# Optimization experiments

Hardware: AMD Instinct MI355X
Metric: run time of the kernel (lower is better)

The kernel has to match this reference:

```python
import jax, jax.numpy as jnp
import numpy as np

NU, NS, NT = 200000, 100000, 100000
N = NS + NU + NT          # node order: [source items | users | target items]
D = 32                    # embedding_size
K = 3                     # graph_layer_K
DK = D * (K + 1)          # 128, concat of all propagation layers
META = 64                 # meta_dim
B = 2048                  # batch
L = 50                    # padded history length
NNZ = 2000000             # nnz of normalized adjacency


def setup_inputs() -> dict:
    key = jax.random.key(0)
    ks = jax.random.split(key, 32)
    f = lambda i, shape, s=0.05: jax.random.normal(ks[i], shape, jnp.float32) * s
    z = lambda shape: jnp.zeros(shape, jnp.float32)
    return dict(
        u=jax.random.randint(ks[0], (B,), 0, NU, jnp.int32),
        si=jax.random.randint(ks[1], (B,), 0, NS, jnp.int32),
        ti=jax.random.randint(ks[2], (B,), 0, NT, jnp.int32),
        src_seq=jax.random.randint(ks[3], (NU, L), 0, NS, jnp.int32),
        tgt_seq=jax.random.randint(ks[4], (NU, L), 0, NT, jnp.int32),
        adj_rows=jax.random.randint(ks[5], (NNZ,), 0, N, jnp.int32),
        adj_cols=jax.random.randint(ks[6], (NNZ,), 0, N, jnp.int32),
        adj_vals=jax.random.uniform(ks[7], (NNZ,), jnp.float32) * 0.1,
        user_emb=f(8, (NU, D), 0.1),
        item_s_emb=f(9, (NS, D), 0.1),
        item_t_emb=f(10, (NT, D), 0.1),
        attn_s_w1=f(11, (D, D)), attn_s_b1=z((D,)), attn_s_w2=f(12, (D, 1)),
        attn_t_w1=f(13, (D, D)), attn_t_b1=z((D,)), attn_t_w2=f(14, (D, 1)),
        dec_ss_w1=f(15, (D, META)), dec_ss_b1=z((META,)),
        dec_ss_w2=f(16, (META, DK * DK), 0.02), dec_ss_b2=z((DK * DK,)),
        dec_tt_w1=f(17, (D, META)), dec_tt_b1=z((META,)),
        dec_tt_w2=f(18, (META, DK * DK), 0.02), dec_tt_b2=z((DK * DK,)),
        mlp_s_w1=f(19, (2 * DK, 128)), mlp_s_b1=z((128,)),
        mlp_s_w2=f(20, (128, 64)), mlp_s_b2=z((64,)),
        dense_s_w=f(21, (64, 1)), dense_s_b=z((1,)),
        mlp_t_w1=f(22, (2 * DK, 128)), mlp_t_b1=z((128,)),
        mlp_t_w2=f(23, (128, 64)), mlp_t_b2=z((64,)),
        dense_t_w=f(24, (64, 1)), dense_t_b=z((1,)),
    )


def _attn_pool(seq_ids, item_emb, w1, b1, w2):
    # masked attention pooling over padded history; pad id is 0
    e = item_emb[seq_ids]                          # [B,L,D]
    h = jax.nn.relu(e @ w1 + b1)                   # attention_layer_K = 1
    logits = h @ w2                                # [B,L,1], no bias on final layer
    mask = (seq_ids == 0)[..., None].astype(e.dtype)
    att = jax.nn.softmax(logits - mask * 1e8, axis=1)
    return jnp.sum(att * e, axis=1)                # [B,D]


def _meta_decode(his, w1, b1, w2, b2, u_e):
    # meta-generated per-sample DKxDK transform applied to the user embedding
    W = (jax.nn.relu(his @ w1 + b1) @ w2 + b2).reshape(-1, DK, DK)
    return jnp.einsum('bd,bde->be', u_e, W)


def _ncf(x, w1, b1, w2, b2, dw, db):
    h = jax.nn.relu(x @ w1 + b1)
    h = jax.nn.relu(h @ w2 + b2)
    return jax.nn.sigmoid(h @ dw + db)[:, 0]


def reference(u, si, ti, src_seq, tgt_seq, adj_rows, adj_cols, adj_vals,
              user_emb, item_s_emb, item_t_emb,
              attn_s_w1, attn_s_b1, attn_s_w2, attn_t_w1, attn_t_b1, attn_t_w2,
              dec_ss_w1, dec_ss_b1, dec_ss_w2, dec_ss_b2,
              dec_tt_w1, dec_tt_b1, dec_tt_w2, dec_tt_b2,
              mlp_s_w1, mlp_s_b1, mlp_s_w2, mlp_s_b2, dense_s_w, dense_s_b,
              mlp_t_w1, mlp_t_b1, mlp_t_w2, mlp_t_b2, dense_t_w, dense_t_b):
    his_s = _attn_pool(src_seq[u], item_s_emb, attn_s_w1, attn_s_b1, attn_s_w2)
    his_t = _attn_pool(tgt_seq[u], item_t_emb, attn_t_w1, attn_t_b1, attn_t_w2)

    # 'raw' graph encoder: K hops of sparse A @ E over [item_s | user | item_t]
    emb = jnp.concatenate([item_s_emb, user_emb, item_t_emb], axis=0)  # [N,D]
    all_emb = [emb]
    for _ in range(K):
        emb = jax.ops.segment_sum(adj_vals[:, None] * emb[adj_cols], adj_rows,
                                  num_segments=N)
        all_emb.append(emb)
    all_e = jnp.concatenate(all_emb, axis=1)       # [N, DK]

    si_e = all_e[si]                               # source items: rows [0, NS)
    u_e = all_e[NS + u]                            # users: rows [NS, NS+NU)
    ti_e = all_e[NS + NU + ti]                     # target items

    u_ss = _meta_decode(his_s, dec_ss_w1, dec_ss_b1, dec_ss_w2, dec_ss_b2, u_e)
    u_tt = _meta_decode(his_t, dec_tt_w1, dec_tt_b1, dec_tt_w2, dec_tt_b2, u_e)

    pred_s = _ncf(jnp.concatenate([u_ss, si_e], -1),
                  mlp_s_w1, mlp_s_b1, mlp_s_w2, mlp_s_b2, dense_s_w, dense_s_b)
    pred_t = _ncf(jnp.concatenate([u_tt, ti_e], -1),
                  mlp_t_w1, mlp_t_b1, mlp_t_w2, mlp_t_b2, dense_t_w, dense_t_b)
    return jnp.stack([pred_s, pred_t])             # [2, B]
```

## Files before the change

### kernel.cpp

```cpp
#include <hip/hip_runtime.h>
#include <hip/hip_bf16.h>

#define NU_ 200000
#define NS_ 100000
#define NT_ 100000
#define NN_ (NS_ + NU_ + NT_)
#define D_ 32
#define DK_ 128
#define META_ 64
#define B_ 2048
#define L_ 50
#define NNZ_ 2000000
#define GK_ 8192

#define RPB_ 391
#define NB_ 1024
#define STAGE_CAP_ 4096
#define CAPA_ 1280
#define CAPB_ 512

#define SB_EMB_   6250
#define IN4_SLOT3_ 100096
#define IN4_MARKS_ 50048
#define IN4_E3C_   49152
#define IN4_TOT_  (IN4_SLOT3_ + IN4_MARKS_ + IN4_E3C_)
#define SB_INIT_  ((IN4_TOT_ + 2048 + 255) / 256)
#define SB_ATT0_  0
#define SB_W2C0_  1024
#define SB_EMB0_  2048
#define SB_INIT0_ (SB_EMB0_ + SB_EMB_)
#define SB_GRID_  (SB_INIT0_ + SB_INIT_)

#define PB_GATHER_ 192
#define PB_TOT_    (PB_GATHER_ + 1024)

#define NCF_TILE_ 16

typedef __attribute__((ext_vector_type(8))) short bf16x8;
typedef __attribute__((ext_vector_type(4))) float f32x4;

__device__ inline unsigned bfpack(float a, float b) {
    unsigned r;
    asm("v_cvt_pk_bf16_f32 %0, %1, %2" : "=v"(r) : "v"(a), "v"(b));
    return r;
}
__device__ inline float bf2f(short s) {
    return __uint_as_float(((unsigned)(unsigned short)s) << 16);
}

__global__ __launch_bounds__(256) void setup_kernel(
    const float* __restrict__ item_s, const float* __restrict__ user_e,
    const float* __restrict__ item_t, unsigned short* __restrict__ tab,
    int* __restrict__ slot3, int* __restrict__ marks ,
    float* __restrict__ E3c, int* __restrict__ bcurA, int* __restrict__ bcurB,
    const int* __restrict__ u,
    const int* __restrict__ seq_s, const int* __restrict__ seq_t,
    const float* __restrict__ aw1_s, const float* __restrict__ ab1_s,
    const float* __restrict__ aw2_s,
    const float* __restrict__ aw1_t, const float* __restrict__ ab1_t,
    const float* __restrict__ aw2_t,
    float* __restrict__ his_s, float* __restrict__ his_t,
    const float* __restrict__ dw2_s, const float* __restrict__ dw2_t,
    unsigned short* __restrict__ o_s, unsigned short* __restrict__ o_t)
{
    __shared__ float w1t[1024];
    __shared__ float b1s[32];
    __shared__ float w2s[32];
    __shared__ float att[4][64];
    __shared__ int   ids[4][52];

    int bid = blockIdx.x, t = threadIdx.x;
    if (bid < SB_W2C0_) {
        int aid = bid;
        int dom = aid >> 9;
        const int* seq = dom ? seq_t : seq_s;
        const float* emb = dom ? item_t : item_s;
        const float* w1 = dom ? aw1_t : aw1_s;
        const float* b1 = dom ? ab1_t : ab1_s;
        const float* w2 = dom ? aw2_t : aw2_s;
        float* out = dom ? his_t : his_s;

        for (int idx = t; idx < 1024; idx += 256)
            w1t[(idx & 31) * 32 + (idx >> 5)] = w1[idx];
        if (t < 32) { b1s[t] = b1[t]; w2s[t] = w2[t]; }
        __syncthreads();

        int w = t >> 6, l = t & 63;
        int b = (aid & 511) * 4 + w;
        int uid = u[b];
        int lq = (l < L_) ? l : (L_ - 1);
        int id = seq[uid * L_ + lq];
        const float4* ep = (const float4*)(emb + (size_t)id * 32);
        float4 e4[8];
        #pragma unroll
        for (int q = 0; q < 8; q++) e4[q] = ep[q];
        float acc = 0.f;
        #pragma unroll
        for (int i = 0; i < 32; i++) {
            float hi = b1s[i];
            const float4* wr = (const float4*)(w1t + i * 32);
            #pragma unroll
            for (int jq = 0; jq < 8; jq++) {
                float4 wf = wr[jq];
                hi += e4[jq].x*wf.x + e4[jq].y*wf.y + e4[jq].z*wf.z + e4[jq].w*wf.w;
            }
            acc += fmaxf(hi, 0.f) * w2s[i];
        }
        float logit = (l < L_) ? (acc - (id == 0 ? 1e8f : 0.f)) : -1e30f;
        float m = logit;
        for (int off = 32; off > 0; off >>= 1) m = fmaxf(m, __shfl_down(m, off, 64));
        m = __shfl(m, 0, 64);
        float ex = (l < L_) ? expf(logit - m) : 0.f;
        float s = ex;
        for (int off = 32; off > 0; off >>= 1) s += __shfl_down(s, off, 64);
        s = __shfl(s, 0, 64);
        att[w][l] = ex / s;
        if (l < L_) ids[w][l] = id;
        __syncthreads();
        {
            int d = l & 31, half = l >> 5;
            int q0 = half * 25;
            float o = 0.f;
            #pragma unroll
            for (int q = 0; q < 25; q++) {
                int qq = q0 + q;
                o += att[w][qq] * emb[(size_t)ids[w][qq] * 32 + d];
            }
            o += __shfl_xor(o, 32, 64);
            if (l < 32) out[b * 32 + l] = o;
        }
    } else if (bid < SB_EMB0_) {
        int b3 = bid - SB_W2C0_;
        int dom = b3 >> 9, sub = b3 & 511;
        const float* w2 = dom ? dw2_t : dw2_s;
        unsigned short* o = dom ? o_t : o_s;
        int tid = sub * 256 + t;
        int nn = tid & 127, k8 = tid >> 7;
        float v[8];
        #pragma unroll
        for (int i = 0; i < 8; i++) v[i] = w2[(size_t)(k8 * 8 + i) * 128 + nn];
        uint4 r;
        r.x = bfpack(v[0], v[1]); r.y = bfpack(v[2], v[3]);
        r.z = bfpack(v[4], v[5]); r.w = bfpack(v[6], v[7]);
        *(uint4*)(o + (size_t)nn * GK_ + k8 * 8) = r;
    } else if (bid < SB_INIT0_) {
        int tid = (bid - SB_EMB0_) * 256 + t;
        int row = tid >> 2, seg = tid & 3;
        const float* src;
        if (row < NS_)            src = item_s + (size_t)row * 32;
        else if (row < NS_ + NU_) src = user_e + (size_t)(row - NS_) * 32;
        else                      src = item_t + (size_t)(row - NS_ - NU_) * 32;
        const float4* sp = (const float4*)(src + seg * 8);
        float4 a = sp[0], b = sp[1];
        uint4 r;
        r.x = bfpack(a.x, a.y); r.y = bfpack(a.z, a.w);
        r.z = bfpack(b.x, b.y); r.w = bfpack(b.z, b.w);
        *(uint4*)(tab + (size_t)row * 32 + seg * 8) = r;
    } else {
        int idx = (bid - SB_INIT0_) * 256 + t;
        if (idx < IN4_SLOT3_) {
            ((int4*)slot3)[idx] = make_int4(-1, -1, -1, -1);
        } else if (idx < IN4_SLOT3_ + IN4_MARKS_) {
            ((int4*)marks)[idx - IN4_SLOT3_] = make_int4(0, 0, 0, 0);
        } else if (idx < IN4_TOT_) {
            ((int4*)E3c)[idx - IN4_SLOT3_ - IN4_MARKS_] = make_int4(0, 0, 0, 0);
        } else {
            int c = idx - IN4_TOT_;
            if (c < NB_)            bcurA[c] = c * CAPA_;
            else if (c < 2 * NB_)   bcurB[c - NB_] = (c - NB_) * CAPB_;
        }
    }
}

__global__ __launch_bounds__(256) void mark_seeds(
    const int* __restrict__ u, const int* __restrict__ si, const int* __restrict__ ti,
    int* __restrict__ slot3, unsigned char* __restrict__ mark1,
    unsigned char* __restrict__ mark2)
{
    int n = blockIdx.x * 256 + threadIdx.x;
    if (n >= 3 * B_) return;
    int which = n >> 11, b = n & (B_ - 1);
    int row = (which == 0) ? si[b] : (which == 1) ? NS_ + u[b] : NS_ + NU_ + ti[b];
    slot3[row] = n;
    mark1[row] = 1;
    mark2[row] = 1;
}

__global__ __launch_bounds__(256) void mark_pass(
    const int* __restrict__ rows, const int* __restrict__ cols,
    const int* __restrict__ slot3, const unsigned char* __restrict__ msrc,
    unsigned char* __restrict__ mdst, int use_slot)
{
    int j = blockIdx.x * 256 + threadIdx.x;
    if (j >= NNZ_) return;
    int r = rows[j];
    bool cond = use_slot ? (slot3[r] >= 0) : (msrc[r] != 0);
    if (cond) mdst[cols[j]] = 1;
}

__global__ __launch_bounds__(512) void partition_edges(
    const int* __restrict__ rows, const int* __restrict__ cols,
    const float* __restrict__ vals,
    const unsigned char* __restrict__ mark1, const unsigned char* __restrict__ mark2,
    int* __restrict__ bcurA, int* __restrict__ bcurB,
    int2* __restrict__ partA, int2* __restrict__ partB)
{
    __shared__ int hist[NB_], sstart[NB_], sbase[NB_], scur[NB_];
    __shared__ int2 stage[STAGE_CAP_];
    __shared__ unsigned short stageb[STAGE_CAP_];
    __shared__ int stotal;

    int t = threadIdx.x;
    for (int i = t; i < NB_; i += 512) hist[i] = 0;
    __syncthreads();

    int base = blockIdx.x * 8192;
    int mybkt[16]; int2 mye[16]; unsigned myB = 0;
    #pragma unroll
    for (int i = 0; i < 16; i++) {
        int j = base + i * 512 + t;
        mybkt[i] = -1;
        if (j < NNZ_) {
            int r = rows[j];
            if (mark1[r]) {
                int bb = r / RPB_;
                int lr = r - bb * RPB_;
                mye[i] = make_int2((lr << 19) | cols[j], __float_as_int(vals[j]));
                mybkt[i] = bb;
                if (mark2[r]) myB |= (1u << i);
                atomicAdd(&hist[bb], 1);
            }
        }
    }
    __syncthreads();
    for (int i = t; i < NB_; i += 512) sstart[i] = hist[i];
    __syncthreads();
    for (int off = 1; off < NB_; off <<= 1) {
        int x0 = (t >= off) ? sstart[t - off] : 0;
        int x1 = (t + 512 >= off) ? sstart[t + 512 - off] : 0;
        __syncthreads();
        sstart[t] += x0; sstart[t + 512] += x1;
        __syncthreads();
    }
    if (t == 0) stotal = sstart[NB_ - 1];
    __syncthreads();
    int tot = stotal;
    for (int i = t; i < NB_; i += 512) {
        int cnt = hist[i];
        sstart[i] -= cnt;
        sbase[i] = cnt ? atomicAdd(&bcurA[i], cnt) : 0;
        scur[i] = 0;
    }
    __syncthreads();

    if (tot <= STAGE_CAP_) {
        #pragma unroll
        for (int i = 0; i < 16; i++) {
            int bb = mybkt[i];
            if (bb >= 0) {
                int p = atomicAdd(&scur[bb], 1);
                int s = sstart[bb] + p;
                stage[s] = mye[i];
                stageb[s] = (unsigned short)bb;
            }
        }
        __syncthreads();
        for (int i = t; i < tot; i += 512) {
            int bb = stageb[i];
            int pos = sbase[bb] + (i - sstart[bb]);
            if (pos < (bb + 1) * CAPA_) partA[pos] = stage[i];
        }
    } else {
        #pragma unroll
        for (int i = 0; i < 16; i++) {
            int bb = mybkt[i];
            if (bb >= 0) {
                int p = atomicAdd(&scur[bb], 1);
                int pos = sbase[bb] + p;
                if (pos < (bb + 1) * CAPA_) partA[pos] = mye[i];
            }
        }
    }
    __syncthreads();
    for (int i = t; i < NB_; i += 512) hist[i] = 0;
    __syncthreads();
    #pragma unroll
    for (int i = 0; i < 16; i++)
        if (myB & (1u << i)) atomicAdd(&hist[mybkt[i]], 1);
    __syncthreads();
    for (int i = t; i < NB_; i += 512) {
        sbase[i] = hist[i] ? atomicAdd(&bcurB[i], hist[i]) : 0;
        scur[i] = 0;
    }
    __syncthreads();
    #pragma unroll
    for (int i = 0; i < 16; i++) {
        if (myB & (1u << i)) {
            int bb = mybkt[i];
            int p = atomicAdd(&scur[bb], 1);
            int pos = sbase[bb] + p;
            if (pos < (bb + 1) * CAPB_) partB[pos] = mye[i];
        }
    }
}

__global__ __launch_bounds__(512) void hop_csr(
    const int* __restrict__ bcur, const int2* __restrict__ part, int cap,
    const unsigned short* __restrict__ tab,
    const unsigned char* __restrict__ markw,
    const int* __restrict__ fgate,
    float* __restrict__ yf, unsigned short* __restrict__ ybf)
{
    __shared__ int2 sorted[CAPA_];
    __shared__ int cnt[RPB_];
    __shared__ int scanb[512];

    int t = threadIdx.x;
    int bkt = blockIdx.x;
    int e0 = bkt * cap;
    int n = bcur[bkt] - e0;
    if (n > cap) n = cap;

    int2 mye[3]; int myl[3];
    #pragma unroll
    for (int i = 0; i < 3; i++) {
        int j = i * 512 + t;
        myl[i] = -1;
        if (j < n) {
            mye[i] = part[e0 + j];
            myl[i] = (mye[i].x >> 19) & 0x3FF;
        }
    }
    for (int i = t; i < RPB_; i += 512) cnt[i] = 0;
    __syncthreads();
    #pragma unroll
    for (int i = 0; i < 3; i++)
        if (myl[i] >= 0) atomicAdd(&cnt[myl[i]], 1);
    __syncthreads();
    scanb[t] = (t < RPB_) ? cnt[t] : 0;
    __syncthreads();
    for (int off = 1; off < 512; off <<= 1) {
        int x = (t >= off) ? scanb[t - off] : 0;
        __syncthreads();
        scanb[t] += x;
        __syncthreads();
    }
    if (t < RPB_) cnt[t] = scanb[t] - cnt[t];
    __syncthreads();
    #pragma unroll
    for (int i = 0; i < 3; i++)
        if (myl[i] >= 0) {
            int p2 = atomicAdd(&cnt[myl[i]], 1);
            sorted[p2] = mye[i];
        }
    __syncthreads();
    int chunk = t & 3;
    int row0 = bkt * RPB_;
    for (int r = t >> 2; r < RPB_; r += 128) {
        int grow = row0 + r;
        if (grow >= NN_ || !markw[grow]) continue;
        int eb = (r == 0) ? 0 : scanb[r - 1];
        int ee = scanb[r];
        float racc[8] = {0.f, 0.f, 0.f, 0.f, 0.f, 0.f, 0.f, 0.f};
        for (int e = eb; e < ee; e++) {
            int2 ed = sorted[e];
            int col = ed.x & 0x7FFFF;
            float vv = __int_as_float(ed.y);
            bf16x8 x = *(const bf16x8*)(tab + (size_t)col * 32 + chunk * 8);
            #pragma unroll
            for (int k = 0; k < 8; k++) racc[k] += vv * bf2f(x[k]);
        }
        float4 o0 = {racc[0], racc[1], racc[2], racc[3]};
        float4 o1 = {racc[4], racc[5], racc[6], racc[7]};
        if (!fgate || fgate[grow] >= 0) {
            float4* yp = (float4*)(yf + (size_t)grow * 32 + chunk * 8);
            yp[0] = o0; yp[1] = o1;
        }
        if (ybf) {
            uint4 pk;
            pk.x = bfpack(o0.x, o0.y); pk.y = bfpack(o0.z, o0.w);
            pk.z = bfpack(o1.x, o1.y); pk.w = bfpack(o1.z, o1.w);
            *(uint4*)(ybf + (size_t)grow * 32 + chunk * 8) = pk;
        }
    }
}

__global__ __launch_bounds__(256) void hop3_part(
    const int* __restrict__ bcurB, const int2* __restrict__ partB,
    const int* __restrict__ slot3,
    const float* __restrict__ E2, float* __restrict__ E3c)
{
    int t = threadIdx.x;
    int bkt = blockIdx.x;
    int e0 = bkt * CAPB_;
    int e1 = bcurB[bkt];
    int emax = e0 + CAPB_;
    if (e1 > emax) e1 = emax;
    int c = t & 7;
    for (int i = e0 + (t >> 3); i < e1; i += 32) {
        int2 e = partB[i];
        int lr = (e.x >> 19) & 0x3FF;
        int s = slot3[bkt * RPB_ + lr];
        if (s < 0) continue;
        int col = e.x & 0x7FFFF;
        float v = __int_as_float(e.y);
        float4 xv = ((const float4*)E2)[(size_t)col * 8 + c];
        float* p = E3c + (size_t)s * 32 + c * 4;
        unsafeAtomicAdd(p + 0, v * xv.x);
        unsafeAtomicAdd(p + 1, v * xv.y);
        unsafeAtomicAdd(p + 2, v * xv.z);
        unsafeAtomicAdd(p + 3, v * xv.w);
    }
}

__global__ __launch_bounds__(256) void prep_kernel(
    const float* __restrict__ E1, const float* __restrict__ E2,
    const float* __restrict__ E3c, const int* __restrict__ slot3,
    const int* __restrict__ u, const int* __restrict__ si, const int* __restrict__ ti,
    const float* __restrict__ user_emb, const float* __restrict__ item_s,
    const float* __restrict__ item_t,
    float* __restrict__ u_e, float* __restrict__ si_e, float* __restrict__ ti_e,
    const float* __restrict__ his_s, const float* __restrict__ his_t,
    const float* __restrict__ dw1_s, const float* __restrict__ db1_s,
    const float* __restrict__ dw1_t, const float* __restrict__ db1_t,
    float* __restrict__ h_s, float* __restrict__ h_t)
{
    int bid = blockIdx.x, t = threadIdx.x;
    if (bid < PB_GATHER_) {
        int tid = bid * 256 + t;
        if (tid >= 3 * B_ * 8) return;
        int n = tid >> 3, c = tid & 7;
        int which = n >> 11, b = n & (B_ - 1);
        int row;
        const float4* base0;
        float* outp;
        if (which == 0)      { int id = si[b]; row = id;             base0 = (const float4*)item_s + (size_t)id * 8; outp = si_e; }
        else if (which == 1) { int id = u[b];  row = NS_ + id;       base0 = (const float4*)user_emb + (size_t)id * 8; outp = u_e; }
        else                 { int id = ti[b]; row = NS_ + NU_ + id; base0 = (const float4*)item_t + (size_t)id * 8; outp = ti_e; }
        float4 k0 = base0[c];
        float4 k1 = ((const float4*)E1)[(size_t)row * 8 + c];
        float4 k2 = ((const float4*)E2)[(size_t)row * 8 + c];
        float4 k3 = ((const float4*)E3c)[(size_t)slot3[row] * 8 + c];
        float4* orow = (float4*)(outp + (size_t)b * 128);
        orow[0 * 8 + c] = k0;
        orow[1 * 8 + c] = k1;
        orow[2 * 8 + c] = k2;
        orow[3 * 8 + c] = k3;
    } else {
        int b2 = bid - PB_GATHER_;
        int dom = b2 >> 9, sub = b2 & 511;
        const float* his = dom ? his_t : his_s;
        const float* w1  = dom ? dw1_t : dw1_s;
        const float* b1  = dom ? db1_t : db1_s;
        float* h         = dom ? h_t   : h_s;
        int b = sub * 4 + (t >> 6);
        int m = t & 63;
        float acc = b1[m];
        #pragma unroll
        for (int j = 0; j < 32; j++) acc += his[b * 32 + j] * w1[j * 64 + m];
        h[b * 64 + m] = fmaxf(acc, 0.f);
    }
}

__global__ __launch_bounds__(256) void meta_gemm(
    const float* __restrict__ h_s, const float* __restrict__ h_t,
    const float* __restrict__ ue,
    const unsigned short* __restrict__ w2t_s, const unsigned short* __restrict__ w2t_t,
    float* __restrict__ P)
{
    __shared__ unsigned short As[64 * 72];
    __shared__ unsigned short Bs[128 * 72];

    int mt = blockIdx.x & 31, dom = blockIdx.x >> 5;
    int ks = blockIdx.y;
    const float* h = dom ? h_t : h_s;
    const unsigned short* w2t = dom ? w2t_t : w2t_s;

    int t = threadIdx.x;
    int ar = t >> 2, aseg = t & 3;
    int bn = t >> 1, bhalf = t & 1;
    int w = t >> 6, lane = t & 63;
    int quad = lane >> 4, l16 = lane & 15;
    int wm = (w & 1) * 32, wn = (w >> 1) * 64;

    f32x4 acc[8];
    #pragma unroll
    for (int i = 0; i < 8; i++) { acc[i][0]=0.f; acc[i][1]=0.f; acc[i][2]=0.f; acc[i][3]=0.f; }

    for (int ch = 0; ch < 16; ch++) {
        int kb = ks * 1024 + ch * 64;
        __syncthreads();
        {
            int gm = mt * 64 + ar;
            int m_idx = kb >> 7;
            int d0 = (kb & 127) + aseg * 16;
            float hv = h[gm * 64 + m_idx];
            const float4* up = (const float4*)(ue + (size_t)gm * 128 + d0);
            float4 x0 = up[0], x1 = up[1], x2 = up[2], x3 = up[3];
            uint4 A0, A1;
            A0.x = bfpack(hv*x0.x, hv*x0.y); A0.y = bfpack(hv*x0.z, hv*x0.w);
            A0.z = bfpack(hv*x1.x, hv*x1.y); A0.w = bfpack(hv*x1.z, hv*x1.w);
            A1.x = bfpack(hv*x2.x, hv*x2.y); A1.y = bfpack(hv*x2.z, hv*x2.w);
            A1.z = bfpack(hv*x3.x, hv*x3.y); A1.w = bfpack(hv*x3.z, hv*x3.w);
            uint4* sa = (uint4*)(As + ar * 72 + aseg * 16);
            sa[0] = A0; sa[1] = A1;
        }
        {
            const uint4* gb = (const uint4*)(w2t + (size_t)bn * GK_ + kb + bhalf * 32);
            uint4* sb = (uint4*)(Bs + bn * 72 + bhalf * 32);
            sb[0] = gb[0]; sb[1] = gb[1]; sb[2] = gb[2]; sb[3] = gb[3];
        }
        __syncthreads();
        #pragma unroll
        for (int kk = 0; kk < 2; kk++) {
            int ko = kk * 32 + quad * 8;
            bf16x8 a0 = *(const bf16x8*)(As + (wm + l16) * 72 + ko);
            bf16x8 a1 = *(const bf16x8*)(As + (wm + 16 + l16) * 72 + ko);
            #pragma unroll
            for (int nt = 0; nt < 4; nt++) {
                bf16x8 bfr = *(const bf16x8*)(Bs + (wn + nt * 16 + l16) * 72 + ko);
                acc[nt]     = __builtin_amdgcn_mfma_f32_16x16x32_bf16(a0, bfr, acc[nt],     0, 0, 0);
                acc[4 + nt] = __builtin_amdgcn_mfma_f32_16x16x32_bf16(a1, bfr, acc[4 + nt], 0, 0, 0);
            }
        }
    }
    float* op = P + ((size_t)dom * 8 + ks) * B_ * 128;
    #pragma unroll
    for (int ma = 0; ma < 2; ma++)
        #pragma unroll
        for (int nt = 0; nt < 4; nt++) {
            int row = mt * 64 + wm + ma * 16 + quad * 4;
            int col = wn + nt * 16 + l16;
            f32x4 v = acc[ma * 4 + nt];
            op[(size_t)(row + 0) * 128 + col] = v[0];
            op[(size_t)(row + 1) * 128 + col] = v[1];
            op[(size_t)(row + 2) * 128 + col] = v[2];
            op[(size_t)(row + 3) * 128 + col] = v[3];
        }
}

__global__ __launch_bounds__(512) void ncf_kernel(
    const float* __restrict__ P, const float* __restrict__ u_e,
    const float* __restrict__ b2_s, const float* __restrict__ b2_t,
    const float* __restrict__ si_e, const float* __restrict__ ti_e,
    const float* __restrict__ w1_s, const float* __restrict__ b1_s,
    const float* __restrict__ w2_s, const float* __restrict__ bb2_s,
    const float* __restrict__ dw_s, const float* __restrict__ db_s,
    const float* __restrict__ w1_t, const float* __restrict__ b1_t,
    const float* __restrict__ w2_t, const float* __restrict__ bb2_t,
    const float* __restrict__ dw_t, const float* __restrict__ db_t,
    float* __restrict__ out)
{
    int tile = blockIdx.x, dom = blockIdx.y, t = threadIdx.x;
    int b0 = tile * NCF_TILE_;
    const float* Pd     = P + (size_t)dom * 8 * B_ * 128;
    const float* b2meta = dom ? b2_t : b2_s;
    const float* pair_e = dom ? ti_e : si_e;
    const float* w1 = dom ? w1_t : w1_s;
    const float* b1 = dom ? b1_t : b1_s;
    const float* w2 = dom ? w2_t : w2_s;
    const float* bb2 = dom ? bb2_t : bb2_s;
    const float* dw = dom ? dw_t : dw_s;
    const float* db = dom ? db_t : db_s;

    __shared__ float ues[NCF_TILE_ * 128];
    __shared__ float xs[NCF_TILE_ * 256];
    __shared__ float h1s[NCF_TILE_ * 128];
    __shared__ float h2s[NCF_TILE_ * 64];

    {
        float4 v = ((const float4*)(u_e + (size_t)b0 * 128))[t];
        ((float4*)ues)[t] = v;
        float4 pv = ((const float4*)(pair_e + (size_t)b0 * 128))[t];
        int s = t >> 5, c4 = t & 31;
        ((float4*)(xs + s * 256 + 128))[c4] = pv;
    }
    __syncthreads();

    int j = t & 127, g = t >> 7;
    {
        float acc[4];
        #pragma unroll
        for (int ss = 0; ss < 4; ss++) {
            int b = b0 + g * 4 + ss;
            float a = 0.f;
            #pragma unroll
            for (int ks = 0; ks < 8; ks++)
                a += Pd[(size_t)ks * B_ * 128 + (size_t)b * 128 + j];
            acc[ss] = a;
        }
        for (int dc = 0; dc < 32; dc++) {
            float wa = b2meta[(dc * 4 + 0) * 128 + j];
            float wb = b2meta[(dc * 4 + 1) * 128 + j];
            float wc = b2meta[(dc * 4 + 2) * 128 + j];
            float wd = b2meta[(dc * 4 + 3) * 128 + j];
            #pragma unroll
            for (int ss = 0; ss < 4; ss++) {
                float4 uv = ((const float4*)(ues + (g * 4 + ss) * 128))[dc];
                acc[ss] += uv.x * wa + uv.y * wb + uv.z * wc + uv.w * wd;
            }
        }
        #pragma unroll
        for (int ss = 0; ss < 4; ss++) xs[(g * 4 + ss) * 256 + j] = acc[ss];
    }
    __syncthreads();

    {
        float b1v = b1[j];
        float acc[4] = {b1v, b1v, b1v, b1v};
        for (int kc = 0; kc < 64; kc++) {
            float wa = w1[(kc * 4 + 0) * 128 + j];
            float wb = w1[(kc * 4 + 1) * 128 + j];
            float wc = w1[(kc * 4 + 2) * 128 + j];
            float wd = w1[(kc * 4 + 3) * 128 + j];
            #pragma unroll
            for (int ss = 0; ss < 4; ss++) {
                float4 xv = ((const float4*)(xs + (g * 4 + ss) * 256))[kc];
                acc[ss] += xv.x * wa + xv.y * wb + xv.z * wc + xv.w * wd;
            }
        }
        #pragma unroll
        for (int ss = 0; ss < 4; ss++)
            h1s[(g * 4 + ss) * 128 + j] = fmaxf(acc[ss], 0.f);
    }
    __syncthreads();

    {
        int m = t & 63, g2 = t >> 6;
        float bv = bb2[m];
        float acc[2] = {bv, bv};
        for (int kc = 0; kc < 32; kc++) {
            float wa = w2[(kc * 4 + 0) * 64 + m];
            float wb = w2[(kc * 4 + 1) * 64 + m];
            float wc = w2[(kc * 4 + 2) * 64 + m];
            float wd = w2[(kc * 4 + 3) * 64 + m];
            #pragma unroll
            for (int ss = 0; ss < 2; ss++) {
                float4 hv = ((const float4*)(h1s + (g2 * 2 + ss) * 128))[kc];
                acc[ss] += hv.x * wa + hv.y * wb + hv.z * wc + hv.w * wd;
            }
        }
        #pragma unroll
        for (int ss = 0; ss < 2; ss++)
            h2s[(g2 * 2 + ss) * 64 + m] = fmaxf(acc[ss], 0.f);
    }
    __syncthreads();

    {
        int s = t >> 5, l = t & 31;
        float sum = h2s[s * 64 + l] * dw[l] + h2s[s * 64 + 32 + l] * dw[32 + l];
        #pragma unroll
        for (int off = 16; off > 0; off >>= 1) sum += __shfl_down(sum, off, 32);
        if (l == 0) {
            float z = sum + db[0];
            out[(size_t)dom * B_ + b0 + s] = 1.f / (1.f + expf(-z));
        }
    }
}

extern "C" void kernel_launch(void* const* d_in, const int* in_sizes, int n_in,
                              void* d_out, int out_size, void* d_ws, size_t ws_size,
                              hipStream_t stream)
{
    const int*   u          = (const int*)  d_in[0];
    const int*   si         = (const int*)  d_in[1];
    const int*   ti         = (const int*)  d_in[2];
    const int*   src_seq    = (const int*)  d_in[3];
    const int*   tgt_seq    = (const int*)  d_in[4];
    const int*   adj_rows   = (const int*)  d_in[5];
    const int*   adj_cols   = (const int*)  d_in[6];
    const float* adj_vals   = (const float*)d_in[7];
    const float* user_emb   = (const float*)d_in[8];
    const float* item_s_emb = (const float*)d_in[9];
    const float* item_t_emb = (const float*)d_in[10];
    const float* attn_s_w1  = (const float*)d_in[11];
    const float* attn_s_b1  = (const float*)d_in[12];
    const float* attn_s_w2  = (const float*)d_in[13];
    const float* attn_t_w1  = (const float*)d_in[14];
    const float* attn_t_b1  = (const float*)d_in[15];
    const float* attn_t_w2  = (const float*)d_in[16];
    const float* dec_ss_w1  = (const float*)d_in[17];
    const float* dec_ss_b1  = (const float*)d_in[18];
    const float* dec_ss_w2  = (const float*)d_in[19];
    const float* dec_ss_b2  = (const float*)d_in[20];
    const float* dec_tt_w1  = (const float*)d_in[21];
    const float* dec_tt_b1  = (const float*)d_in[22];
    const float* dec_tt_w2  = (const float*)d_in[23];
    const float* dec_tt_b2  = (const float*)d_in[24];
    const float* mlp_s_w1   = (const float*)d_in[25];
    const float* mlp_s_b1   = (const float*)d_in[26];
    const float* mlp_s_w2   = (const float*)d_in[27];
    const float* mlp_s_b2   = (const float*)d_in[28];
    const float* dense_s_w  = (const float*)d_in[29];
    const float* dense_s_b  = (const float*)d_in[30];
    const float* mlp_t_w1   = (const float*)d_in[31];
    const float* mlp_t_b1   = (const float*)d_in[32];
    const float* mlp_t_w2   = (const float*)d_in[33];
    const float* mlp_t_b2   = (const float*)d_in[34];
    const float* dense_t_w  = (const float*)d_in[35];
    const float* dense_t_b  = (const float*)d_in[36];

    char* p = (char*)d_ws;
    float* E1    = (float*)p;              p += (size_t)NN_ * 32 * 4;
    float* E2    = (float*)p;              p += (size_t)NN_ * 32 * 4;
    unsigned short* Ebf  = (unsigned short*)p; p += (size_t)NN_ * 32 * 2;
    unsigned short* E1bf = (unsigned short*)p; p += (size_t)NN_ * 32 * 2;
    int2*  partA = (int2*)p;               p += (size_t)NB_ * CAPA_ * 8;
    int2*  partB = (int2*)p;               p += (size_t)NB_ * CAPB_ * 8;
    int*   slot3 = (int*)p;                p += (size_t)400384 * 4;
    int*   marks = (int*)p;
    unsigned char* mark1 = (unsigned char*)p; p += 400384;
    unsigned char* mark2 = (unsigned char*)p; p += 400384;
    float* E3c   = (float*)p;              p += (size_t)3 * B_ * 32 * 4;
    int*   bcurA = (int*)p;                p += NB_ * 4;
    int*   bcurB = (int*)p;                p += NB_ * 4;
    float* his_s = (float*)p;              p += (size_t)B_ * 32 * 4;
    float* his_t = (float*)p;              p += (size_t)B_ * 32 * 4;
    float* u_e   = (float*)p;              p += (size_t)B_ * 128 * 4;
    float* si_e  = (float*)p;              p += (size_t)B_ * 128 * 4;
    float* ti_e  = (float*)p;              p += (size_t)B_ * 128 * 4;
    float* h_s   = (float*)p;              p += (size_t)B_ * 64 * 4;
    float* h_t   = (float*)p;              p += (size_t)B_ * 64 * 4;
    float* P     = (float*)p;              p += (size_t)2 * 8 * B_ * 128 * 4;
    unsigned short* w2t_s = (unsigned short*)p; p += (size_t)128 * GK_ * 2;
    unsigned short* w2t_t = (unsigned short*)p; p += (size_t)128 * GK_ * 2;

    int nnzBlocks = (NNZ_ + 255) / 256;

    setup_kernel<<<SB_GRID_, 256, 0, stream>>>(item_s_emb, user_emb, item_t_emb,
                                               Ebf, slot3, marks, E3c, bcurA, bcurB,
                                               u, src_seq, tgt_seq,
                                               attn_s_w1, attn_s_b1, attn_s_w2,
                                               attn_t_w1, attn_t_b1, attn_t_w2,
                                               his_s, his_t,
                                               dec_ss_w2, dec_tt_w2, w2t_s, w2t_t);
    mark_seeds<<<24, 256, 0, stream>>>(u, si, ti, slot3, mark1, mark2);
    mark_pass<<<nnzBlocks, 256, 0, stream>>>(adj_rows, adj_cols, slot3, mark2, mark2, 1);
    mark_pass<<<nnzBlocks, 256, 0, stream>>>(adj_rows, adj_cols, slot3, mark2, mark1, 0);
    partition_edges<<<245, 512, 0, stream>>>(adj_rows, adj_cols, adj_vals,
                                             mark1, mark2, bcurA, bcurB, partA, partB);
    hop_csr<<<NB_, 512, 0, stream>>>(bcurA, partA, CAPA_, Ebf,  mark1, slot3, E1, E1bf);
    hop_csr<<<NB_, 512, 0, stream>>>(bcurB, partB, CAPB_, E1bf, mark2, nullptr, E2, nullptr);
    hop3_part<<<NB_, 256, 0, stream>>>(bcurB, partB, slot3, E2, E3c);
    prep_kernel<<<PB_TOT_, 256, 0, stream>>>(E1, E2, E3c, slot3, u, si, ti,
                                             user_emb, item_s_emb, item_t_emb,
                                             u_e, si_e, ti_e,
                                             his_s, his_t,
                                             dec_ss_w1, dec_ss_b1,
                                             dec_tt_w1, dec_tt_b1, h_s, h_t);
    meta_gemm<<<dim3(64, 8), 256, 0, stream>>>(h_s, h_t, u_e, w2t_s, w2t_t, P);
    ncf_kernel<<<dim3(B_ / NCF_TILE_, 2), 512, 0, stream>>>(P, u_e, dec_ss_b2, dec_tt_b2,
                                                si_e, ti_e,
                                                mlp_s_w1, mlp_s_b1, mlp_s_w2, mlp_s_b2,
                                                dense_s_w, dense_s_b,
                                                mlp_t_w1, mlp_t_b1, mlp_t_w2, mlp_t_b2,
                                                dense_t_w, dense_t_b,
                                                (float*)d_out);
}
```

Baseline: 411.9 us.

## Reduce split-K partials with atomics, vectorize mark pass, shrink partition blocks

meta_gemm now accumulates its 8 split-K partials directly into a single zeroed P0 buffer using float atomics, instead of writing 8 separate partial slabs that ncf_kernel then summed. P0 is zeroed in setup_kernel. mark_pass reads rows and cols as int4, handling four edges per thread. partition_edges processes 4096 edges per block instead of 8192, which doubles the grid and lets it always use the LDS staging path. The atomics make the summation order nondeterministic and add atomic traffic to global memory.

```diff
diff --git a/kernel.cpp b/kernel.cpp
--- a/kernel.cpp
+++ b/kernel.cpp
@@ -18,12 +18,17 @@
 #define STAGE_CAP_ 4096
 #define CAPA_ 1280
 #define CAPB_ 512
+#define PEB_  4096
+#define PE_GRID_ ((NNZ_ + PEB_ - 1) / PEB_)
 
 #define SB_EMB_   6250
 #define IN4_SLOT3_ 100096
 #define IN4_MARKS_ 50048
 #define IN4_E3C_   49152
-#define IN4_TOT_  (IN4_SLOT3_ + IN4_MARKS_ + IN4_E3C_)
+#define IN4_P0_    131072
+#define IN4_M1_   (IN4_SLOT3_ + IN4_MARKS_)
+#define IN4_M2_   (IN4_M1_ + IN4_E3C_)
+#define IN4_TOT_  (IN4_M2_ + IN4_P0_)
 #define SB_INIT_  ((IN4_TOT_ + 2048 + 255) / 256)
 #define SB_ATT0_  0
 #define SB_W2C0_  1024
@@ -52,7 +57,8 @@
     const float* __restrict__ item_s, const float* __restrict__ user_e,
     const float* __restrict__ item_t, unsigned short* __restrict__ tab,
     int* __restrict__ slot3, int* __restrict__ marks ,
-    float* __restrict__ E3c, int* __restrict__ bcurA, int* __restrict__ bcurB,
+    float* __restrict__ E3c, float* __restrict__ P0,
+    int* __restrict__ bcurA, int* __restrict__ bcurB,
     const int* __restrict__ u,
     const int* __restrict__ seq_s, const int* __restrict__ seq_t,
     const float* __restrict__ aw1_s, const float* __restrict__ ab1_s,
@@ -160,10 +166,12 @@
         int idx = (bid - SB_INIT0_) * 256 + t;
         if (idx < IN4_SLOT3_) {
             ((int4*)slot3)[idx] = make_int4(-1, -1, -1, -1);
-        } else if (idx < IN4_SLOT3_ + IN4_MARKS_) {
+        } else if (idx < IN4_M1_) {
             ((int4*)marks)[idx - IN4_SLOT3_] = make_int4(0, 0, 0, 0);
+        } else if (idx < IN4_M2_) {
+            ((int4*)E3c)[idx - IN4_M1_] = make_int4(0, 0, 0, 0);
         } else if (idx < IN4_TOT_) {
-            ((int4*)E3c)[idx - IN4_SLOT3_ - IN4_MARKS_] = make_int4(0, 0, 0, 0);
+            ((int4*)P0)[idx - IN4_M2_] = make_int4(0, 0, 0, 0);
         } else {
             int c = idx - IN4_TOT_;
             if (c < NB_)            bcurA[c] = c * CAPA_;
@@ -191,11 +199,21 @@
     const int* __restrict__ slot3, const unsigned char* __restrict__ msrc,
     unsigned char* __restrict__ mdst, int use_slot)
 {
-    int j = blockIdx.x * 256 + threadIdx.x;
-    if (j >= NNZ_) return;
-    int r = rows[j];
-    bool cond = use_slot ? (slot3[r] >= 0) : (msrc[r] != 0);
-    if (cond) mdst[cols[j]] = 1;
+    int j4 = blockIdx.x * 256 + threadIdx.x;
+    if (j4 >= NNZ_ / 4) return;
+    int4 r = ((const int4*)rows)[j4];
+    int4 c = ((const int4*)cols)[j4];
+    if (use_slot) {
+        if (slot3[r.x] >= 0) mdst[c.x] = 1;
+        if (slot3[r.y] >= 0) mdst[c.y] = 1;
+        if (slot3[r.z] >= 0) mdst[c.z] = 1;
+        if (slot3[r.w] >= 0) mdst[c.w] = 1;
+    } else {
+        if (msrc[r.x]) mdst[c.x] = 1;
+        if (msrc[r.y]) mdst[c.y] = 1;
+        if (msrc[r.z]) mdst[c.z] = 1;
+        if (msrc[r.w]) mdst[c.w] = 1;
+    }
 }
 
 __global__ __launch_bounds__(512) void partition_edges(
@@ -214,10 +232,10 @@
     for (int i = t; i < NB_; i += 512) hist[i] = 0;
     __syncthreads();
 
-    int base = blockIdx.x * 8192;
-    int mybkt[16]; int2 mye[16]; unsigned myB = 0;
-    #pragma unroll
-    for (int i = 0; i < 16; i++) {
+    int base = blockIdx.x * PEB_;
+    int mybkt[8]; int2 mye[8]; unsigned myB = 0;
+    #pragma unroll
+    for (int i = 0; i < 8; i++) {
         int j = base + i * 512 + t;
         mybkt[i] = -1;
         if (j < NNZ_) {
@@ -253,39 +271,27 @@
     }
     __syncthreads();
 
-    if (tot <= STAGE_CAP_) {
-        #pragma unroll
-        for (int i = 0; i < 16; i++) {
-            int bb = mybkt[i];
-            if (bb >= 0) {
-                int p = atomicAdd(&scur[bb], 1);
-                int s = sstart[bb] + p;
-                stage[s] = mye[i];
-                stageb[s] = (unsigned short)bb;
-            }
-        }
-        __syncthreads();
-        for (int i = t; i < tot; i += 512) {
-            int bb = stageb[i];
-            int pos = sbase[bb] + (i - sstart[bb]);
-            if (pos < (bb + 1) * CAPA_) partA[pos] = stage[i];
-        }
-    } else {
-        #pragma unroll
-        for (int i = 0; i < 16; i++) {
-            int bb = mybkt[i];
-            if (bb >= 0) {
-                int p = atomicAdd(&scur[bb], 1);
-                int pos = sbase[bb] + p;
-                if (pos < (bb + 1) * CAPA_) partA[pos] = mye[i];
-            }
-        }
+    #pragma unroll
+    for (int i = 0; i < 8; i++) {
+        int bb = mybkt[i];
+        if (bb >= 0) {
+            int p = atomicAdd(&scur[bb], 1);
+            int s = sstart[bb] + p;
+            stage[s] = mye[i];
+            stageb[s] = (unsigned short)bb;
+        }
+    }
+    __syncthreads();
+    for (int i = t; i < tot; i += 512) {
+        int bb = stageb[i];
+        int pos = sbase[bb] + (i - sstart[bb]);
+        if (pos < (bb + 1) * CAPA_) partA[pos] = stage[i];
     }
     __syncthreads();
     for (int i = t; i < NB_; i += 512) hist[i] = 0;
     __syncthreads();
     #pragma unroll
-    for (int i = 0; i < 16; i++)
+    for (int i = 0; i < 8; i++)
         if (myB & (1u << i)) atomicAdd(&hist[mybkt[i]], 1);
     __syncthreads();
     for (int i = t; i < NB_; i += 512) {
@@ -294,7 +300,7 @@
     }
     __syncthreads();
     #pragma unroll
-    for (int i = 0; i < 16; i++) {
+    for (int i = 0; i < 8; i++) {
         if (myB & (1u << i)) {
             int bb = mybkt[i];
             int p = atomicAdd(&scur[bb], 1);
@@ -466,7 +472,7 @@
     const float* __restrict__ h_s, const float* __restrict__ h_t,
     const float* __restrict__ ue,
     const unsigned short* __restrict__ w2t_s, const unsigned short* __restrict__ w2t_t,
-    float* __restrict__ P)
+    float* __restrict__ P0)
 {
     __shared__ unsigned short As[64 * 72];
     __shared__ unsigned short Bs[128 * 72];
@@ -524,7 +530,7 @@
             }
         }
     }
-    float* op = P + ((size_t)dom * 8 + ks) * B_ * 128;
+    float* op = P0 + (size_t)dom * B_ * 128;
     #pragma unroll
     for (int ma = 0; ma < 2; ma++)
         #pragma unroll
@@ -532,15 +538,15 @@
             int row = mt * 64 + wm + ma * 16 + quad * 4;
             int col = wn + nt * 16 + l16;
             f32x4 v = acc[ma * 4 + nt];
-            op[(size_t)(row + 0) * 128 + col] = v[0];
-            op[(size_t)(row + 1) * 128 + col] = v[1];
-            op[(size_t)(row + 2) * 128 + col] = v[2];
-            op[(size_t)(row + 3) * 128 + col] = v[3];
+            unsafeAtomicAdd(&op[(size_t)(row + 0) * 128 + col], v[0]);
+            unsafeAtomicAdd(&op[(size_t)(row + 1) * 128 + col], v[1]);
+            unsafeAtomicAdd(&op[(size_t)(row + 2) * 128 + col], v[2]);
+            unsafeAtomicAdd(&op[(size_t)(row + 3) * 128 + col], v[3]);
         }
 }
 
 __global__ __launch_bounds__(512) void ncf_kernel(
-    const float* __restrict__ P, const float* __restrict__ u_e,
+    const float* __restrict__ P0, const float* __restrict__ u_e,
     const float* __restrict__ b2_s, const float* __restrict__ b2_t,
     const float* __restrict__ si_e, const float* __restrict__ ti_e,
     const float* __restrict__ w1_s, const float* __restrict__ b1_s,
@@ -553,7 +559,7 @@
 {
     int tile = blockIdx.x, dom = blockIdx.y, t = threadIdx.x;
     int b0 = tile * NCF_TILE_;
-    const float* Pd     = P + (size_t)dom * 8 * B_ * 128;
+    const float* Pd     = P0 + (size_t)dom * B_ * 128;
     const float* b2meta = dom ? b2_t : b2_s;
     const float* pair_e = dom ? ti_e : si_e;
     const float* w1 = dom ? w1_t : w1_s;
@@ -583,11 +589,7 @@
         #pragma unroll
         for (int ss = 0; ss < 4; ss++) {
             int b = b0 + g * 4 + ss;
-            float a = 0.f;
-            #pragma unroll
-            for (int ks = 0; ks < 8; ks++)
-                a += Pd[(size_t)ks * B_ * 128 + (size_t)b * 128 + j];
-            acc[ss] = a;
+            acc[ss] = Pd[(size_t)b * 128 + j];
         }
         for (int dc = 0; dc < 32; dc++) {
             float wa = b2meta[(dc * 4 + 0) * 128 + j];
@@ -721,24 +723,23 @@
     float* ti_e  = (float*)p;              p += (size_t)B_ * 128 * 4;
     float* h_s   = (float*)p;              p += (size_t)B_ * 64 * 4;
     float* h_t   = (float*)p;              p += (size_t)B_ * 64 * 4;
-    float* P     = (float*)p;              p += (size_t)2 * 8 * B_ * 128 * 4;
+    float* P0    = (float*)p;              p += (size_t)2 * B_ * 128 * 4;
     unsigned short* w2t_s = (unsigned short*)p; p += (size_t)128 * GK_ * 2;
     unsigned short* w2t_t = (unsigned short*)p; p += (size_t)128 * GK_ * 2;
 
-    int nnzBlocks = (NNZ_ + 255) / 256;
-
     setup_kernel<<<SB_GRID_, 256, 0, stream>>>(item_s_emb, user_emb, item_t_emb,
-                                               Ebf, slot3, marks, E3c, bcurA, bcurB,
+                                               Ebf, slot3, marks, E3c, P0, bcurA, bcurB,
                                                u, src_seq, tgt_seq,
                                                attn_s_w1, attn_s_b1, attn_s_w2,
                                                attn_t_w1, attn_t_b1, attn_t_w2,
                                                his_s, his_t,
                                                dec_ss_w2, dec_tt_w2, w2t_s, w2t_t);
     mark_seeds<<<24, 256, 0, stream>>>(u, si, ti, slot3, mark1, mark2);
-    mark_pass<<<nnzBlocks, 256, 0, stream>>>(adj_rows, adj_cols, slot3, mark2, mark2, 1);
-    mark_pass<<<nnzBlocks, 256, 0, stream>>>(adj_rows, adj_cols, slot3, mark2, mark1, 0);
-    partition_edges<<<245, 512, 0, stream>>>(adj_rows, adj_cols, adj_vals,
-                                             mark1, mark2, bcurA, bcurB, partA, partB);
+    int m4Blocks = (NNZ_ / 4 + 255) / 256;
+    mark_pass<<<m4Blocks, 256, 0, stream>>>(adj_rows, adj_cols, slot3, mark2, mark2, 1);
+    mark_pass<<<m4Blocks, 256, 0, stream>>>(adj_rows, adj_cols, slot3, mark2, mark1, 0);
+    partition_edges<<<PE_GRID_, 512, 0, stream>>>(adj_rows, adj_cols, adj_vals,
+                                                  mark1, mark2, bcurA, bcurB, partA, partB);
     hop_csr<<<NB_, 512, 0, stream>>>(bcurA, partA, CAPA_, Ebf,  mark1, slot3, E1, E1bf);
     hop_csr<<<NB_, 512, 0, stream>>>(bcurB, partB, CAPB_, E1bf, mark2, nullptr, E2, nullptr);
     hop3_part<<<NB_, 256, 0, stream>>>(bcurB, partB, slot3, E2, E3c);
@@ -748,8 +749,8 @@
                                              his_s, his_t,
                                              dec_ss_w1, dec_ss_b1,
                                              dec_tt_w1, dec_tt_b1, h_s, h_t);
-    meta_gemm<<<dim3(64, 8), 256, 0, stream>>>(h_s, h_t, u_e, w2t_s, w2t_t, P);
-    ncf_kernel<<<dim3(B_ / NCF_TILE_, 2), 512, 0, stream>>>(P, u_e, dec_ss_b2, dec_tt_b2,
+    meta_gemm<<<dim3(64, 8), 256, 0, stream>>>(h_s, h_t, u_e, w2t_s, w2t_t, P0);
+    ncf_kernel<<<dim3(B_ / NCF_TILE_, 2), 512, 0, stream>>>(P0, u_e, dec_ss_b2, dec_tt_b2,
                                                 si_e, ti_e,
                                                 mlp_s_w1, mlp_s_b1, mlp_s_w2, mlp_s_b2,
                                                 dense_s_w, dense_s_b,
```

Measured after the change: 413.6 us. No clear change (+0.4%).
